# Kernel tuning notes

Hardware: AMD Instinct MI355X
Metric: run time of the kernel (lower is better)

Reference implementation:

```python
import jax, jax.numpy as jnp
import numpy as np

N_NODES = 50000
N_EDGES = 640000
DIM_IN = 128
DIM_OUT = 32
NUM_GRAPHS = 64


def setup_inputs() -> dict:
    key = jax.random.key(0)
    ks = jax.random.split(key, 8)
    x = jax.random.normal(ks[0], (N_NODES, DIM_IN), dtype=jnp.float32)
    edge_index = jax.random.randint(ks[1], (2, N_EDGES), 0, N_NODES, dtype=jnp.int64)
    batch = jnp.sort(jax.random.randint(ks[2], (N_NODES,), 0, NUM_GRAPHS, dtype=jnp.int64))
    s = 1.0 / np.sqrt(DIM_IN)
    W1 = jax.random.normal(ks[3], (DIM_IN, DIM_IN), dtype=jnp.float32) * s
    b1 = jnp.zeros((DIM_IN,), dtype=jnp.float32)
    W2 = jax.random.normal(ks[4], (DIM_IN, DIM_IN), dtype=jnp.float32) * s
    b2 = jnp.zeros((DIM_IN,), dtype=jnp.float32)
    Wh = jax.random.normal(ks[5], (DIM_IN, DIM_OUT), dtype=jnp.float32) * s
    bh = jnp.zeros((DIM_OUT,), dtype=jnp.float32)
    return {"x": x, "edge_index": edge_index, "batch": batch,
            "W1": W1, "b1": b1, "W2": W2, "b2": b2, "Wh": Wh, "bh": bh}


def _gcn_conv(x, src, dst, norm, W, b):
    # GCNConv: h = x @ W; out[i] = sum_{(j->i)} norm_e * h[j] + b
    h = x @ W
    msg = h[src] * norm[:, None]                      # [E+N, D] gather + scale
    out = jax.ops.segment_sum(msg, dst, num_segments=x.shape[0])
    return out + b


def reference(x, edge_index, batch, W1, b1, W2, b2, Wh, bh):
    n = x.shape[0]
    loops = jnp.arange(n, dtype=edge_index.dtype)
    src = jnp.concatenate([edge_index[0], loops])     # add self-loops
    dst = jnp.concatenate([edge_index[1], loops])
    # symmetric normalization: deg^{-1/2}[src] * deg^{-1/2}[dst]
    deg = jax.ops.segment_sum(jnp.ones_like(dst, dtype=x.dtype), dst, num_segments=n)
    dinv = jnp.where(deg > 0, jax.lax.rsqrt(deg), 0.0)
    norm = dinv[src] * dinv[dst]

    h = jax.nn.relu(_gcn_conv(x, src, dst, norm, W1, b1))   # dropout = identity (eval)
    h = jax.nn.relu(_gcn_conv(h, src, dst, norm, W2, b2))
    pooled = jax.ops.segment_sum(h, batch, num_segments=NUM_GRAPHS)  # global_add_pool
    logits = pooled @ Wh + bh
    return jax.nn.log_softmax(logits, axis=1)
```

## Files before the change

### kernel.cpp

```cpp
#include <hip/hip_runtime.h>
#include <hip/hip_bf16.h>
#include <math.h>

#define N_NODES 50000
#define N_EDGES 640000
#define DIM     128
#define NGRAPH  64
#define DOUT    32
#define CAP     64
#define CNT_BLOCKS 2500
#define LDSS 136
#define LDSF 132

typedef unsigned short u16;
typedef __attribute__((ext_vector_type(8))) short bf16x8;
typedef __attribute__((ext_vector_type(4))) float f32x4;

__device__ __forceinline__ u16 f2bf(float f) {
    unsigned u = __float_as_uint(f);
    return (u16)((u + 0x7FFFu + ((u >> 16) & 1u)) >> 16);
}
__device__ __forceinline__ float bf2f(u16 h) {
    return __uint_as_float(((unsigned)h) << 16);
}
__device__ __forceinline__ short2 cvt2(float x, float y) {
    __hip_bfloat162 h = __float22bfloat162_rn(make_float2(x, y));
    return *(short2*)&h;
}
__device__ __forceinline__ void upk(unsigned u, float& lo, float& hi) {
    lo = __uint_as_float(u << 16);
    hi = __uint_as_float(u & 0xFFFF0000u);
}

__global__ __launch_bounds__(256) void k_fill_cvt(const int* __restrict__ src,
                                                  const int* __restrict__ dst,
                                                  int* __restrict__ cnt,
                                                  int* __restrict__ bucket,
                                                  const float* __restrict__ W1,
                                                  const float* __restrict__ W2,
                                                  u16* __restrict__ W1s,
                                                  u16* __restrict__ W2s,
                                                  float* __restrict__ pooled) {
    int b = blockIdx.x;
    if (b < CNT_BLOCKS) {
        int e = b * 256 + threadIdx.x;
        int d = dst[e];
        int pos = atomicAdd(&cnt[d], 1);
        bucket[d * CAP + pos] = src[e];
    } else if (b < CNT_BLOCKS + 128) {
        int t = (b - CNT_BLOCKS) * 256 + threadIdx.x;
        int r = t & 16383;
        int j = r & 7, lane = (r >> 3) & 63, kc = (r >> 9) & 3, nt = r >> 11;
        int k = kc * 32 + (lane >> 4) * 8 + j;
        int n = nt * 16 + (lane & 15);
        if (t < 16384) W1s[r] = f2bf(W1[k * 128 + n]);
        else           W2s[r] = f2bf(W2[k * 128 + n]);
    } else {
        int t = (b - CNT_BLOCKS - 128) * 256 + threadIdx.x;
        if (t < NGRAPH * DIM) pooled[t] = 0.f;
    }
}

__global__ __launch_bounds__(256) void k_gemm1(const float* __restrict__ X,
                                               const u16* __restrict__ Ws,
                                               const int* __restrict__ cnt,
                                               u16* __restrict__ Y) {
    int wv   = threadIdx.x >> 6;
    int lane = threadIdx.x & 63;
    int row0 = blockIdx.x * 64 + wv * 16;
    int m    = lane & 15;
    int quad = lane >> 4;
    int ar = min(row0 + m, N_NODES - 1);
    const float* Arow = X + (size_t)ar * DIM;
    bf16x8 a[4];
#pragma unroll
    for (int kc = 0; kc < 4; ++kc) {
        const float4* p4 = (const float4*)(Arow + kc * 32 + quad * 8);
        float4 p = p4[0], q = p4[1];
        short2 s0 = cvt2(p.x, p.y), s1 = cvt2(p.z, p.w);
        short2 s2 = cvt2(q.x, q.y), s3 = cvt2(q.z, q.w);
        bf16x8 av;
        av[0] = s0.x; av[1] = s0.y; av[2] = s1.x; av[3] = s1.y;
        av[4] = s2.x; av[5] = s2.y; av[6] = s3.x; av[7] = s3.y;
        a[kc] = av;
    }
    float di[4];
#pragma unroll
    for (int r = 0; r < 4; ++r) {
        int rr = row0 + quad * 4 + r;
        di[r] = (rr < N_NODES) ? rsqrtf((float)(cnt[rr] + 1)) : 0.f;
    }
#pragma unroll
    for (int nt = 0; nt < 8; ++nt) {
        f32x4 acc = {0.f, 0.f, 0.f, 0.f};
#pragma unroll
        for (int kc = 0; kc < 4; ++kc) {
            bf16x8 b = *(const bf16x8*)(Ws + ((size_t)(nt * 4 + kc) * 64 + lane) * 8);
            acc = __builtin_amdgcn_mfma_f32_16x16x32_bf16(a[kc], b, acc, 0, 0, 0);
        }
        int col = nt * 16 + m;
#pragma unroll
        for (int r = 0; r < 4; ++r) {
            int rr = row0 + quad * 4 + r;
            if (rr < N_NODES) Y[(size_t)rr * DIM + col] = f2bf(acc[r] * di[r]);
        }
    }
}

__global__ __launch_bounds__(256) void k_agg_gemm(const u16* __restrict__ H,
                                                  const int* __restrict__ bucket,
                                                  const int* __restrict__ cnt,
                                                  const float* __restrict__ bias,
                                                  const u16* __restrict__ Ws,
                                                  u16* __restrict__ Y) {
    __shared__ u16 As[16][LDSS];
    int tid    = threadIdx.x;
    int nloc   = tid >> 4;
    int lane16 = tid & 15;
    int node   = blockIdx.x * 16 + nloc;

    int deg = cnt[node];
    int e0 = node * CAP, e1 = e0 + deg;
    const uint4* H4 = (const uint4*)H;
    uint4 sv = H4[(size_t)node * 16 + lane16];
    float a0[8], a1[8] = {}, a2[8] = {}, a3[8] = {};
    upk(sv.x, a0[0], a0[1]); upk(sv.y, a0[2], a0[3]);
    upk(sv.z, a0[4], a0[5]); upk(sv.w, a0[6], a0[7]);
    for (int e = e0; e < e1; e += 8) {
        int4 c0 = *(const int4*)(bucket + e);
        int4 c1 = *(const int4*)(bucket + e + 4);
        int   idx[8];
        float w[8];
        uint4 v[8];
        idx[0] = c0.x; idx[1] = c0.y; idx[2] = c0.z; idx[3] = c0.w;
        idx[4] = c1.x; idx[5] = c1.y; idx[6] = c1.z; idx[7] = c1.w;
#pragma unroll
        for (int u = 0; u < 8; ++u) {
            bool in = (e + u) < e1;
            w[u]   = in ? 1.f : 0.f;
            idx[u] = in ? idx[u] : 0;
        }
#pragma unroll
        for (int u = 0; u < 8; ++u) v[u] = H4[(size_t)idx[u] * 16 + lane16];
#pragma unroll
        for (int u = 0; u < 8; ++u) {
            float* a = (u & 3) == 0 ? a0 : (u & 3) == 1 ? a1 : (u & 3) == 2 ? a2 : a3;
            float lo, hi;
            upk(v[u].x, lo, hi); a[0] = fmaf(w[u], lo, a[0]); a[1] = fmaf(w[u], hi, a[1]);
            upk(v[u].y, lo, hi); a[2] = fmaf(w[u], lo, a[2]); a[3] = fmaf(w[u], hi, a[3]);
            upk(v[u].z, lo, hi); a[4] = fmaf(w[u], lo, a[4]); a[5] = fmaf(w[u], hi, a[5]);
            upk(v[u].w, lo, hi); a[6] = fmaf(w[u], lo, a[6]); a[7] = fmaf(w[u], hi, a[7]);
        }
    }
    {
        float di = rsqrtf((float)(deg + 1));
        const float4* b4 = (const float4*)bias;
        float4 blo = b4[lane16 * 2], bhi = b4[lane16 * 2 + 1];
        float r0 = fmaxf(di * (a0[0] + a1[0] + a2[0] + a3[0]) + blo.x, 0.f);
        float r1 = fmaxf(di * (a0[1] + a1[1] + a2[1] + a3[1]) + blo.y, 0.f);
        float r2 = fmaxf(di * (a0[2] + a1[2] + a2[2] + a3[2]) + blo.z, 0.f);
        float r3 = fmaxf(di * (a0[3] + a1[3] + a2[3] + a3[3]) + blo.w, 0.f);
        float r4 = fmaxf(di * (a0[4] + a1[4] + a2[4] + a3[4]) + bhi.x, 0.f);
        float r5 = fmaxf(di * (a0[5] + a1[5] + a2[5] + a3[5]) + bhi.y, 0.f);
        float r6 = fmaxf(di * (a0[6] + a1[6] + a2[6] + a3[6]) + bhi.z, 0.f);
        float r7 = fmaxf(di * (a0[7] + a1[7] + a2[7] + a3[7]) + bhi.w, 0.f);
        short2 s0 = cvt2(r0, r1), s1 = cvt2(r2, r3), s2 = cvt2(r4, r5), s3 = cvt2(r6, r7);
        uint4 o;
        o.x = *(unsigned*)&s0; o.y = *(unsigned*)&s1;
        o.z = *(unsigned*)&s2; o.w = *(unsigned*)&s3;
        *(uint4*)(&As[nloc][lane16 * 8]) = o;
    }
    __syncthreads();

    int wv   = tid >> 6;
    int lane = tid & 63;
    int m    = lane & 15;
    int quad = lane >> 4;
    bf16x8 a[4];
#pragma unroll
    for (int kc = 0; kc < 4; ++kc)
        a[kc] = *(const bf16x8*)(&As[m][kc * 32 + quad * 8]);
    float di[4];
#pragma unroll
    for (int r = 0; r < 4; ++r)
        di[r] = rsqrtf((float)(cnt[blockIdx.x * 16 + quad * 4 + r] + 1));
#pragma unroll
    for (int i = 0; i < 2; ++i) {
        int nt = wv * 2 + i;
        f32x4 acc = {0.f, 0.f, 0.f, 0.f};
#pragma unroll
        for (int kc = 0; kc < 4; ++kc) {
            bf16x8 b = *(const bf16x8*)(Ws + ((size_t)(nt * 4 + kc) * 64 + lane) * 8);
            acc = __builtin_amdgcn_mfma_f32_16x16x32_bf16(a[kc], b, acc, 0, 0, 0);
        }
        int col = nt * 16 + m;
#pragma unroll
        for (int r = 0; r < 4; ++r) {
            int rr = blockIdx.x * 16 + quad * 4 + r;
            Y[(size_t)rr * DIM + col] = f2bf(acc[r] * di[r]);
        }
    }
}

__global__ __launch_bounds__(256) void k_agg_pool(const u16* __restrict__ H,
                                                  const int* __restrict__ bucket,
                                                  const int* __restrict__ cnt,
                                                  const float* __restrict__ bias,
                                                  const int* __restrict__ batch,
                                                  float* __restrict__ pooled) {
    __shared__ float As[16][LDSF];
    __shared__ int bs[16];
    int tid  = threadIdx.x;
    int nloc = tid >> 4;
    int lane = tid & 15;
    int node = blockIdx.x * 16 + nloc;

    int deg = cnt[node];
    int e0 = node * CAP, e1 = e0 + deg;
    const uint4* H4 = (const uint4*)H;
    uint4 sv = H4[(size_t)node * 16 + lane];
    float a0[8], a1[8] = {}, a2[8] = {}, a3[8] = {};
    upk(sv.x, a0[0], a0[1]); upk(sv.y, a0[2], a0[3]);
    upk(sv.z, a0[4], a0[5]); upk(sv.w, a0[6], a0[7]);
    for (int e = e0; e < e1; e += 8) {
        int4 c0 = *(const int4*)(bucket + e);
        int4 c1 = *(const int4*)(bucket + e + 4);
        int   idx[8];
        float w[8];
        uint4 v[8];
        idx[0] = c0.x; idx[1] = c0.y; idx[2] = c0.z; idx[3] = c0.w;
        idx[4] = c1.x; idx[5] = c1.y; idx[6] = c1.z; idx[7] = c1.w;
#pragma unroll
        for (int u = 0; u < 8; ++u) {
            bool in = (e + u) < e1;
            w[u]   = in ? 1.f : 0.f;
            idx[u] = in ? idx[u] : 0;
        }
#pragma unroll
        for (int u = 0; u < 8; ++u) v[u] = H4[(size_t)idx[u] * 16 + lane];
#pragma unroll
        for (int u = 0; u < 8; ++u) {
            float* a = (u & 3) == 0 ? a0 : (u & 3) == 1 ? a1 : (u & 3) == 2 ? a2 : a3;
            float lo, hi;
            upk(v[u].x, lo, hi); a[0] = fmaf(w[u], lo, a[0]); a[1] = fmaf(w[u], hi, a[1]);
            upk(v[u].y, lo, hi); a[2] = fmaf(w[u], lo, a[2]); a[3] = fmaf(w[u], hi, a[3]);
            upk(v[u].z, lo, hi); a[4] = fmaf(w[u], lo, a[4]); a[5] = fmaf(w[u], hi, a[5]);
            upk(v[u].w, lo, hi); a[6] = fmaf(w[u], lo, a[6]); a[7] = fmaf(w[u], hi, a[7]);
        }
    }
    {
        float di = rsqrtf((float)(deg + 1));
        const float4* b4 = (const float4*)bias;
        float4 blo = b4[lane * 2], bhi = b4[lane * 2 + 1];
        float4 olo, ohi;
        olo.x = fmaxf(di * (a0[0] + a1[0] + a2[0] + a3[0]) + blo.x, 0.f);
        olo.y = fmaxf(di * (a0[1] + a1[1] + a2[1] + a3[1]) + blo.y, 0.f);
        olo.z = fmaxf(di * (a0[2] + a1[2] + a2[2] + a3[2]) + blo.z, 0.f);
        olo.w = fmaxf(di * (a0[3] + a1[3] + a2[3] + a3[3]) + blo.w, 0.f);
        ohi.x = fmaxf(di * (a0[4] + a1[4] + a2[4] + a3[4]) + bhi.x, 0.f);
        ohi.y = fmaxf(di * (a0[5] + a1[5] + a2[5] + a3[5]) + bhi.y, 0.f);
        ohi.z = fmaxf(di * (a0[6] + a1[6] + a2[6] + a3[6]) + bhi.z, 0.f);
        ohi.w = fmaxf(di * (a0[7] + a1[7] + a2[7] + a3[7]) + bhi.w, 0.f);
        *(float4*)(&As[nloc][lane * 8])     = olo;
        *(float4*)(&As[nloc][lane * 8 + 4]) = ohi;
    }
    if (lane == 0) bs[nloc] = batch[node];
    __syncthreads();

    if (tid < 128) {
        float acc = 0.f;
        int cb = bs[0];
#pragma unroll
        for (int n = 0; n < 16; ++n) {
            int b = bs[n];
            if (b != cb) {
                atomicAdd(&pooled[cb * DIM + tid], acc);
                acc = 0.f; cb = b;
            }
            acc += As[n][tid];
        }
        atomicAdd(&pooled[cb * DIM + tid], acc);
    }
}

__global__ __launch_bounds__(64) void k_head(const float* __restrict__ pooled,
                                             const float* __restrict__ Wh,
                                             const float* __restrict__ bh,
                                             float* __restrict__ out) {
    int g = blockIdx.x;
    int lane = threadIdx.x;
    int c = lane & 31;
    const float* p = pooled + g * DIM;
    float lg = bh[c];
#pragma unroll 8
    for (int k = 0; k < DIM; ++k) lg = fmaf(p[k], Wh[k * DOUT + c], lg);
    float m = lg;
    for (int off = 16; off >= 1; off >>= 1) m = fmaxf(m, __shfl_xor(m, off, 32));
    float ex = expf(lg - m);
    float s = ex;
    for (int off = 16; off >= 1; off >>= 1) s += __shfl_xor(s, off, 32);
    if (lane < 32) out[g * DOUT + c] = lg - m - logf(s);
}

extern "C" void kernel_launch(void* const* d_in, const int* in_sizes, int n_in,
                              void* d_out, int out_size, void* d_ws, size_t ws_size,
                              hipStream_t stream) {
    const float* x     = (const float*)d_in[0];
    const int*   ei    = (const int*)d_in[1];
    const int*   batch = (const int*)d_in[2];
    const float* W1    = (const float*)d_in[3];
    const float* b1    = (const float*)d_in[4];
    const float* W2    = (const float*)d_in[5];
    const float* b2    = (const float*)d_in[6];
    const float* Wh    = (const float*)d_in[7];
    const float* bh    = (const float*)d_in[8];
    float* out = (float*)d_out;
    const int* src = ei;
    const int* dst = ei + N_EDGES;

    char* ws = (char*)d_ws;
    size_t off = 0;
    auto alloc = [&](size_t bytes) {
        void* p = ws + off;
        off += (bytes + 255) & ~(size_t)255;
        return p;
    };
    u16*   bufA   = (u16*) alloc((size_t)N_NODES * DIM * 2);
    u16*   bufB   = (u16*) alloc((size_t)N_NODES * DIM * 2);
    int*   cnt    = (int*) alloc((size_t)N_NODES * 4);
    int*   bucket = (int*) alloc((size_t)N_NODES * CAP * 4);
    u16*   W1s    = (u16*) alloc((size_t)DIM * DIM * 2);
    u16*   W2s    = (u16*) alloc((size_t)DIM * DIM * 2);
    float* pooled = (float*)alloc((size_t)NGRAPH * DIM * 4);
    (void)ws_size; (void)in_sizes; (void)n_in; (void)out_size;

    hipMemsetAsync(cnt, 0, (size_t)N_NODES * 4, stream);

    k_fill_cvt<<<CNT_BLOCKS + 128 + 32, 256, 0, stream>>>(src, dst, cnt, bucket,
                                                          W1, W2, W1s, W2s, pooled);

    k_gemm1   <<<(N_NODES + 63) / 64, 256, 0, stream>>>(x, W1s, cnt, bufA);
    k_agg_gemm<<<N_NODES / 16, 256, 0, stream>>>(bufA, bucket, cnt, b1, W2s, bufB);
    k_agg_pool<<<N_NODES / 16, 256, 0, stream>>>(bufB, bucket, cnt, b2, batch, pooled);

    k_head<<<NGRAPH, 64, 0, stream>>>(pooled, Wh, bh, out);
}
```

Before: 203.4 us.

## Fuse layer-1 GEMM into edge-bucketing kernel, moving source-degree scaling into aggregation

Merges the edge bucket fill, weight conversion, pooled zeroing and the first X@W1 GEMM into one launch. Each GEMM block converts W1 into LDS itself instead of reading a pre-converted global copy. Because the GEMM no longer waits for degree counts, the source-side normalisation moves into the first aggregation, which gathers cnt for each neighbour and applies rsqrt per edge. This removes one kernel launch and its serialisation, and lets the GEMM overlap with the atomic bucket fill. The cost is 32KB of LDS per GEMM block, redundant W1 conversion in every block, and extra per-edge cnt gathers and rsqrt in aggregation.

```diff
diff --git a/kernel.cpp b/kernel.cpp
--- a/kernel.cpp
+++ b/kernel.cpp
@@ -8,9 +8,17 @@
 #define NGRAPH  64
 #define DOUT    32
 #define CAP     64
-#define CNT_BLOCKS 2500
 #define LDSS 136
 #define LDSF 132
+
+#define G_GEMM  782
+#define B_W2    (G_GEMM)
+#define N_W2    64
+#define B_ZERO  (B_W2 + N_W2)
+#define N_ZERO  32
+#define B_FILL  (B_ZERO + N_ZERO)
+#define N_FILL  2500
+#define G_FRONT (B_FILL + N_FILL)
 
 typedef unsigned short u16;
 typedef __attribute__((ext_vector_type(8))) short bf16x8;
@@ -32,78 +40,85 @@
     hi = __uint_as_float(u & 0xFFFF0000u);
 }
 
-__global__ __launch_bounds__(256) void k_fill_cvt(const int* __restrict__ src,
-                                                  const int* __restrict__ dst,
-                                                  int* __restrict__ cnt,
-                                                  int* __restrict__ bucket,
-                                                  const float* __restrict__ W1,
-                                                  const float* __restrict__ W2,
-                                                  u16* __restrict__ W1s,
-                                                  u16* __restrict__ W2s,
-                                                  float* __restrict__ pooled) {
-    int b = blockIdx.x;
-    if (b < CNT_BLOCKS) {
-        int e = b * 256 + threadIdx.x;
-        int d = dst[e];
-        int pos = atomicAdd(&cnt[d], 1);
-        bucket[d * CAP + pos] = src[e];
-    } else if (b < CNT_BLOCKS + 128) {
-        int t = (b - CNT_BLOCKS) * 256 + threadIdx.x;
-        int r = t & 16383;
-        int j = r & 7, lane = (r >> 3) & 63, kc = (r >> 9) & 3, nt = r >> 11;
+__global__ __launch_bounds__(256) void k_front(const float* __restrict__ X,
+                                               const int* __restrict__ src,
+                                               const int* __restrict__ dst,
+                                               int* __restrict__ cnt,
+                                               int* __restrict__ bucket,
+                                               const float* __restrict__ W1,
+                                               const float* __restrict__ W2,
+                                               u16* __restrict__ W2s,
+                                               float* __restrict__ pooled,
+                                               u16* __restrict__ Y) {
+    __shared__ u16 Wl[16384];
+    int b   = blockIdx.x;
+    int tid = threadIdx.x;
+
+    if (b < G_GEMM) {
+        const float4* W14 = (const float4*)W1;
+#pragma unroll
+        for (int i = 0; i < 16; ++i) {
+            int q = i * 256 + tid;
+            float4 vv = W14[q];
+            int base = q * 4;
+            int k = base >> 7, n0 = base & 127;
+            int rb = ((n0 >> 4) * 4 + (k >> 5)) * 512 + ((k & 31) >> 3) * 128
+                   + (k & 7) + (n0 & 15) * 8;
+            Wl[rb]      = f2bf(vv.x);
+            Wl[rb + 8]  = f2bf(vv.y);
+            Wl[rb + 16] = f2bf(vv.z);
+            Wl[rb + 24] = f2bf(vv.w);
+        }
+        int wv   = tid >> 6;
+        int lane = tid & 63;
+        int row0 = b * 64 + wv * 16;
+        int m    = lane & 15;
+        int quad = lane >> 4;
+        int ar = min(row0 + m, N_NODES - 1);
+        const float* Arow = X + (size_t)ar * DIM;
+        bf16x8 a[4];
+#pragma unroll
+        for (int kc = 0; kc < 4; ++kc) {
+            const float4* p4 = (const float4*)(Arow + kc * 32 + quad * 8);
+            float4 p = p4[0], q = p4[1];
+            short2 s0 = cvt2(p.x, p.y), s1 = cvt2(p.z, p.w);
+            short2 s2 = cvt2(q.x, q.y), s3 = cvt2(q.z, q.w);
+            bf16x8 av;
+            av[0] = s0.x; av[1] = s0.y; av[2] = s1.x; av[3] = s1.y;
+            av[4] = s2.x; av[5] = s2.y; av[6] = s3.x; av[7] = s3.y;
+            a[kc] = av;
+        }
+        __syncthreads();
+#pragma unroll
+        for (int nt = 0; nt < 8; ++nt) {
+            f32x4 acc = {0.f, 0.f, 0.f, 0.f};
+#pragma unroll
+            for (int kc = 0; kc < 4; ++kc) {
+                bf16x8 bb = *(const bf16x8*)(&Wl[((nt * 4 + kc) * 64 + lane) * 8]);
+                acc = __builtin_amdgcn_mfma_f32_16x16x32_bf16(a[kc], bb, acc, 0, 0, 0);
+            }
+            int col = nt * 16 + m;
+#pragma unroll
+            for (int r = 0; r < 4; ++r) {
+                int rr = row0 + quad * 4 + r;
+                if (rr < N_NODES) Y[(size_t)rr * DIM + col] = f2bf(acc[r]);
+            }
+        }
+    } else if (b < B_ZERO) {
+        int t = (b - B_W2) * 256 + tid;
+        int j = t & 7, lane = (t >> 3) & 63, kc = (t >> 9) & 3, nt = t >> 11;
         int k = kc * 32 + (lane >> 4) * 8 + j;
         int n = nt * 16 + (lane & 15);
-        if (t < 16384) W1s[r] = f2bf(W1[k * 128 + n]);
-        else           W2s[r] = f2bf(W2[k * 128 + n]);
+        W2s[t] = f2bf(W2[k * 128 + n]);
+    } else if (b < B_FILL) {
+        int t = (b - B_ZERO) * 256 + tid;
+        pooled[t] = 0.f;
     } else {
-        int t = (b - CNT_BLOCKS - 128) * 256 + threadIdx.x;
-        if (t < NGRAPH * DIM) pooled[t] = 0.f;
-    }
-}
-
-__global__ __launch_bounds__(256) void k_gemm1(const float* __restrict__ X,
-                                               const u16* __restrict__ Ws,
-                                               const int* __restrict__ cnt,
-                                               u16* __restrict__ Y) {
-    int wv   = threadIdx.x >> 6;
-    int lane = threadIdx.x & 63;
-    int row0 = blockIdx.x * 64 + wv * 16;
-    int m    = lane & 15;
-    int quad = lane >> 4;
-    int ar = min(row0 + m, N_NODES - 1);
-    const float* Arow = X + (size_t)ar * DIM;
-    bf16x8 a[4];
-#pragma unroll
-    for (int kc = 0; kc < 4; ++kc) {
-        const float4* p4 = (const float4*)(Arow + kc * 32 + quad * 8);
-        float4 p = p4[0], q = p4[1];
-        short2 s0 = cvt2(p.x, p.y), s1 = cvt2(p.z, p.w);
-        short2 s2 = cvt2(q.x, q.y), s3 = cvt2(q.z, q.w);
-        bf16x8 av;
-        av[0] = s0.x; av[1] = s0.y; av[2] = s1.x; av[3] = s1.y;
-        av[4] = s2.x; av[5] = s2.y; av[6] = s3.x; av[7] = s3.y;
-        a[kc] = av;
-    }
-    float di[4];
-#pragma unroll
-    for (int r = 0; r < 4; ++r) {
-        int rr = row0 + quad * 4 + r;
-        di[r] = (rr < N_NODES) ? rsqrtf((float)(cnt[rr] + 1)) : 0.f;
-    }
-#pragma unroll
-    for (int nt = 0; nt < 8; ++nt) {
-        f32x4 acc = {0.f, 0.f, 0.f, 0.f};
-#pragma unroll
-        for (int kc = 0; kc < 4; ++kc) {
-            bf16x8 b = *(const bf16x8*)(Ws + ((size_t)(nt * 4 + kc) * 64 + lane) * 8);
-            acc = __builtin_amdgcn_mfma_f32_16x16x32_bf16(a[kc], b, acc, 0, 0, 0);
-        }
-        int col = nt * 16 + m;
-#pragma unroll
-        for (int r = 0; r < 4; ++r) {
-            int rr = row0 + quad * 4 + r;
-            if (rr < N_NODES) Y[(size_t)rr * DIM + col] = f2bf(acc[r] * di[r]);
-        }
+        int e = (b - B_FILL) * 256 + tid;
+        int d = dst[e];
+        int s = src[e];
+        int pos = atomicAdd(&cnt[d], 1);
+        bucket[d * CAP + pos] = s;
     }
 }
 
@@ -120,18 +135,25 @@
     int node   = blockIdx.x * 16 + nloc;
 
     int deg = cnt[node];
+    float dself = rsqrtf((float)(deg + 1));
     int e0 = node * CAP, e1 = e0 + deg;
     const uint4* H4 = (const uint4*)H;
     uint4 sv = H4[(size_t)node * 16 + lane16];
     float a0[8], a1[8] = {}, a2[8] = {}, a3[8] = {};
-    upk(sv.x, a0[0], a0[1]); upk(sv.y, a0[2], a0[3]);
-    upk(sv.z, a0[4], a0[5]); upk(sv.w, a0[6], a0[7]);
+    {
+        float lo, hi;
+        upk(sv.x, lo, hi); a0[0] = dself * lo; a0[1] = dself * hi;
+        upk(sv.y, lo, hi); a0[2] = dself * lo; a0[3] = dself * hi;
+        upk(sv.z, lo, hi); a0[4] = dself * lo; a0[5] = dself * hi;
+        upk(sv.w, lo, hi); a0[6] = dself * lo; a0[7] = dself * hi;
+    }
     for (int e = e0; e < e1; e += 8) {
         int4 c0 = *(const int4*)(bucket + e);
         int4 c1 = *(const int4*)(bucket + e + 4);
         int   idx[8];
         float w[8];
         uint4 v[8];
+        int   cd[8];
         idx[0] = c0.x; idx[1] = c0.y; idx[2] = c0.z; idx[3] = c0.w;
         idx[4] = c1.x; idx[5] = c1.y; idx[6] = c1.z; idx[7] = c1.w;
 #pragma unroll
@@ -141,7 +163,11 @@
             idx[u] = in ? idx[u] : 0;
         }
 #pragma unroll
+        for (int u = 0; u < 8; ++u) cd[u] = cnt[idx[u]];
+#pragma unroll
         for (int u = 0; u < 8; ++u) v[u] = H4[(size_t)idx[u] * 16 + lane16];
+#pragma unroll
+        for (int u = 0; u < 8; ++u) w[u] *= rsqrtf((float)(cd[u] + 1));
 #pragma unroll
         for (int u = 0; u < 8; ++u) {
             float* a = (u & 3) == 0 ? a0 : (u & 3) == 1 ? a1 : (u & 3) == 2 ? a2 : a3;
@@ -153,7 +179,7 @@
         }
     }
     {
-        float di = rsqrtf((float)(deg + 1));
+        float di = dself;
         const float4* b4 = (const float4*)bias;
         float4 blo = b4[lane16 * 2], bhi = b4[lane16 * 2 + 1];
         float r0 = fmaxf(di * (a0[0] + a1[0] + a2[0] + a3[0]) + blo.x, 0.f);
@@ -329,17 +355,14 @@
     u16*   bufB   = (u16*) alloc((size_t)N_NODES * DIM * 2);
     int*   cnt    = (int*) alloc((size_t)N_NODES * 4);
     int*   bucket = (int*) alloc((size_t)N_NODES * CAP * 4);
-    u16*   W1s    = (u16*) alloc((size_t)DIM * DIM * 2);
     u16*   W2s    = (u16*) alloc((size_t)DIM * DIM * 2);
     float* pooled = (float*)alloc((size_t)NGRAPH * DIM * 4);
     (void)ws_size; (void)in_sizes; (void)n_in; (void)out_size;
 
     hipMemsetAsync(cnt, 0, (size_t)N_NODES * 4, stream);
 
-    k_fill_cvt<<<CNT_BLOCKS + 128 + 32, 256, 0, stream>>>(src, dst, cnt, bucket,
-                                                          W1, W2, W1s, W2s, pooled);
-
-    k_gemm1   <<<(N_NODES + 63) / 64, 256, 0, stream>>>(x, W1s, cnt, bufA);
+    k_front   <<<G_FRONT, 256, 0, stream>>>(x, src, dst, cnt, bucket, W1, W2,
+                                            W2s, pooled, bufA);
     k_agg_gemm<<<N_NODES / 16, 256, 0, stream>>>(bufA, bucket, cnt, b1, W2s, bufB);
     k_agg_pool<<<N_NODES / 16, 256, 0, stream>>>(bufB, bucket, cnt, b2, batch, pooled);
 
```

After: 197.0 us. 3.2% less time.
